# Kernel tuning notes

Hardware: AMD Instinct MI355X
Metric: run time of the kernel (lower is better)

## Reference

```python
import jax, jax.numpy as jnp
import numpy as np

NUM_HEADS = 12
NUM_LANDMARKS = 64
EPS_REG = 1e-4


def setup_inputs() -> dict:
    key = jax.random.key(0)
    k1, k2, k3 = jax.random.split(key, 3)
    B, N, C = 4, 4096, 768
    x = jax.random.normal(k1, (B, N, C), dtype=jnp.float32)
    w_qkv = jax.random.normal(k2, (3 * C, C), dtype=jnp.float32) * (C ** -0.5)
    w_proj = jax.random.normal(k3, (C, C), dtype=jnp.float32) * (C ** -0.5)
    b_proj = jnp.zeros((C,), dtype=jnp.float32)
    return {"x": x, "w_qkv": w_qkv, "w_proj": w_proj, "b_proj": b_proj}


def _landmark_pool(t, m):
    # t: [B, H, N, D]; assumes N % m == 0 (true for chosen shapes)
    B, H, N, D = t.shape
    seg = N // m
    return t.reshape(B, H, m, seg, D).mean(axis=3)


def reference(x, w_qkv, w_proj, b_proj):
    B, N, C = x.shape
    H = NUM_HEADS
    D = C // H
    m = min(NUM_LANDMARKS, N)
    scale = D ** -0.5

    qkv = x @ w_qkv.T                              # [B, N, 3C]
    qkv = qkv.reshape(B, N, 3, H, D).transpose(2, 0, 3, 1, 4)
    q, k, v = qkv[0], qkv[1], qkv[2]               # [B, H, N, D]

    q_lm = _landmark_pool(q, m)                    # [B, H, m, D]
    k_lm = _landmark_pool(k, m)                    # [B, H, m, D]

    attn_q_km = jax.nn.softmax(jnp.einsum('bhnd,bhmd->bhnm', q, k_lm) * scale, axis=-1)
    attn_qm_km = jax.nn.softmax(jnp.einsum('bhld,bhmd->bhlm', q_lm, k_lm) * scale, axis=-1)
    attn_qm_k = jax.nn.softmax(jnp.einsum('bhmd,bhnd->bhmn', q_lm, k) * scale, axis=-1)

    eye = jnp.eye(m, dtype=attn_qm_km.dtype)
    inv_mid = jnp.linalg.inv(attn_qm_km + EPS_REG * eye)   # [B, H, m, m]

    out = attn_q_km @ (inv_mid @ (attn_qm_k @ v))          # [B, H, N, D]
    out = out.transpose(0, 2, 1, 3).reshape(B, N, C)
    out = out @ w_proj.T + b_proj
    return out
```

## Files before the change

### kernel.cpp

```cpp
#include <hip/hip_runtime.h>

typedef unsigned short u16;
typedef __attribute__((ext_vector_type(8))) short bf16x8;
typedef __attribute__((ext_vector_type(8))) unsigned short u16x8;
typedef __attribute__((ext_vector_type(4))) unsigned short u16x4;
typedef __attribute__((ext_vector_type(4))) float f32x4;

#define NB 4
#define NH 12
#define NSEQ 4096
#define NC 768
#define ND 64
#define NM 64
#define NBH 48

__device__ __forceinline__ float b2f(u16 u){ unsigned v = ((unsigned)u)<<16; return __builtin_bit_cast(float, v); }
__device__ __forceinline__ u16 f2b(float f){ unsigned u = __builtin_bit_cast(unsigned, f); u = u + 0x7FFFu + ((u>>16)&1u); return (u16)(u>>16); }
__device__ __forceinline__ void split2(float f, u16& h, u16& l){
  h = f2b(f);
  l = f2b(f - b2f(h));
}

typedef const __attribute__((address_space(1))) unsigned int guint;
typedef __attribute__((address_space(3))) unsigned int luint;
__device__ __forceinline__ void gload16(const void* g, void* l){
  __builtin_amdgcn_global_load_lds((guint*)g, (luint*)l, 16, 0, 0);
}

__device__ __forceinline__ f32x4 mfma16x16(bf16x8 a, bf16x8 b, f32x4 c){
  return __builtin_amdgcn_mfma_f32_16x16x32_bf16(a, b, c, 0, 0, 0);
}

#define NX4 3145728
#define NWQ4 442368
#define NWP4 147456
__global__ __launch_bounds__(256) void k_split3(const float* __restrict__ x, const float* __restrict__ wq,
                                                const float* __restrict__ wp,
                                                u16* __restrict__ xh, u16* __restrict__ xl,
                                                u16* __restrict__ wqh, u16* __restrict__ wql,
                                                u16* __restrict__ wph, u16* __restrict__ wpl){
  int i = blockIdx.x*256 + threadIdx.x;
  const float* src; u16 *dh, *dl; int j;
  if (i < NX4){ src = x; dh = xh; dl = xl; j = i; }
  else if (i < NX4+NWQ4){ src = wq; dh = wqh; dl = wql; j = i - NX4; }
  else if (i < NX4+NWQ4+NWP4){ src = wp; dh = wph; dl = wpl; j = i - NX4 - NWQ4; }
  else return;
  f32x4 v = ((const f32x4*)src)[j];
  u16x4 hh, ll;
  #pragma unroll
  for (int e=0;e<4;++e){ u16 hb, lb; split2(v[e], hb, lb); hh[e]=hb; ll[e]=lb; }
  ((u16x4*)dh)[j] = hh; ((u16x4*)dl)[j] = ll;
}


__global__ __launch_bounds__(256) void k_qkv(const u16* __restrict__ xh, const u16* __restrict__ xl,
                                             const u16* __restrict__ wh, const u16* __restrict__ wl,
                                             u16* __restrict__ qh, u16* __restrict__ ql,
                                             u16* __restrict__ kh, u16* __restrict__ kl,
                                             u16* __restrict__ vTh, u16* __restrict__ vTl,
                                             float* __restrict__ qlmf, float* __restrict__ klmf,
                                             u16* __restrict__ qlmh, u16* __restrict__ qlml,
                                             u16* __restrict__ klmh, u16* __restrict__ klml){
  __shared__ u16 lds[32768];
  const int K = NC;
  int tid = threadIdx.x, wave = tid>>6, lane = tid&63;
  int wm = wave>>1, wn = wave&1;
  int bid = blockIdx.x;
  int swz = (bid&7)*288 + (bid>>3);
  int bx = swz % 18, by = swz / 18;
  int m0 = by*128, n0 = bx*128;
  int srow = lane>>3;
  int scol = ((lane&7) ^ srow)*8;
  const u16* src0; u16* dst0;
  if (wave==0){ src0 = xh + (size_t)m0*K; dst0 = lds; }
  else if (wave==1){ src0 = xl + (size_t)m0*K; dst0 = lds+8192; }
  else if (wave==2){ src0 = wh + (size_t)n0*K; dst0 = lds+16384; }
  else            { src0 = wl + (size_t)n0*K; dst0 = lds+24576; }
  f32x4 acc[4][4] = {};
  for (int k0=0; k0<K; k0+=64){
    #pragma unroll
    for (int it=0; it<16; ++it){
      int r = it*8;
      gload16(&src0[(size_t)(r+srow)*K + k0 + scol], &dst0[r*64]);
    }
    __syncthreads();
    #pragma unroll
    for (int kk=0; kk<2; ++kk){
      int sl = ((kk*4 + (lane>>4)) ^ (lane&7))*8;
      bf16x8 a_h[4], a_l[4], b_h[4], b_l[4];
      #pragma unroll
      for (int i=0;i<4;++i){
        int ro = (wm*64+i*16+(lane&15))*64 + sl;
        a_h[i] = *(const bf16x8*)&lds[ro]; a_l[i] = *(const bf16x8*)&lds[8192+ro];
      }
      #pragma unroll
      for (int j=0;j<4;++j){
        int ro = (wn*64+j*16+(lane&15))*64 + sl;
        b_h[j] = *(const bf16x8*)&lds[16384+ro]; b_l[j] = *(const bf16x8*)&lds[24576+ro];
      }
      #pragma unroll
      for (int i=0;i<4;++i)
        #pragma unroll
        for (int j=0;j<4;++j){
          acc[i][j] = mfma16x16(a_h[i], b_h[j], acc[i][j]);
          acc[i][j] = mfma16x16(a_h[i], b_l[j], acc[i][j]);
          acc[i][j] = mfma16x16(a_l[i], b_h[j], acc[i][j]);
        }
    }
    __syncthreads();
  }
  int rb = (lane>>4)*4, cb = lane&15;
  int b_ = m0>>12, nlo = m0&4095;
  if (n0 < 1536){
    int s = n0/768;
    u16* dh = s ? kh : qh;
    u16* dl = s ? kl : ql;
    float* lmf = s ? klmf : qlmf;
    u16* lmh = s ? klmh : qlmh;
    u16* lml = s ? klml : qlml;
    #pragma unroll
    for (int j=0;j<4;++j){
      int gn = n0 + wn*64 + j*16 + cb;
      int rem = gn - s*768; int hd = rem>>6, d = rem&63;
      #pragma unroll
      for (int i=0;i<4;++i)
        #pragma unroll
        for (int r=0;r<4;++r){
          int n = nlo + wm*64 + i*16 + rb + r;
          size_t idx = (((size_t)(b_*NH + hd))*NSEQ + n)*ND + d;
          u16 hb, lb; split2(acc[i][j][r], hb, lb);
          dh[idx] = hb; dl[idx] = lb;
        }
      float tot = 0.f;
      #pragma unroll
      for (int i=0;i<4;++i)
        #pragma unroll
        for (int r=0;r<4;++r) tot += acc[i][j][r];
      tot += __shfl_xor(tot, 16);
      tot += __shfl_xor(tot, 32);
      if (lane < 16){
        int lseg = (nlo>>6) + wm;
        float mean = tot * (1.f/64.f);
        size_t o = (((size_t)(b_*NH + hd))*NM + lseg)*ND + d;
        lmf[o] = mean;
        u16 hb, lb; split2(mean, hb, lb);
        lmh[o] = hb; lml[o] = lb;
      }
    }
  } else {
    const int TS = 136;
    #pragma unroll
    for (int part=0; part<2; ++part){
      __syncthreads();
      #pragma unroll
      for (int j=0;j<4;++j){
        int dcol = wn*64 + j*16 + cb;
        #pragma unroll
        for (int i=0;i<4;++i)
          #pragma unroll
          for (int r=0;r<4;++r){
            int nrow = wm*64 + i*16 + rb + r;
            u16 hb, lb; split2(acc[i][j][r], hb, lb);
            lds[dcol*TS + nrow] = part ? lb : hb;
          }
      }
      __syncthreads();
      int drow = tid>>1, half = (tid&1)*64;
      int remd = (n0 - 1536) + drow;
      int hd = remd>>6, dd = remd&63;
      u16* dst = (part ? vTl : vTh) + (((size_t)(b_*NH + hd))*ND + dd)*NSEQ + nlo + half;
      const u16* srcl = &lds[drow*TS + half];
      #pragma unroll
      for (int e=0;e<8;++e)
        *(u16x8*)(dst + e*8) = *(const u16x8*)(srcl + e*8);
    }
  }
}

__global__ __launch_bounds__(256) void k_proj(const u16* __restrict__ Hh, const u16* __restrict__ Hl,
                                              const u16* __restrict__ wh, const u16* __restrict__ wl,
                                              const float* __restrict__ bias, float* __restrict__ out){
  __shared__ u16 lds[32768];
  const int K = NC;
  int tid = threadIdx.x, wave = tid>>6, lane = tid&63;
  int wm = wave>>1, wn = wave&1;
  int bid = blockIdx.x;
  int swz = (bid&7)*96 + (bid>>3);
  int bx = swz % 6, by = swz / 6;
  int m0 = by*128, n0 = bx*128;
  int srow = lane>>3;
  int scol = ((lane&7) ^ srow)*8;
  const u16* src0; u16* dst0;
  if (wave==0){ src0 = Hh + (size_t)m0*K; dst0 = lds; }
  else if (wave==1){ src0 = Hl + (size_t)m0*K; dst0 = lds+8192; }
  else if (wave==2){ src0 = wh + (size_t)n0*K; dst0 = lds+16384; }
  else            { src0 = wl + (size_t)n0*K; dst0 = lds+24576; }
  f32x4 acc[4][4] = {};
  for (int k0=0; k0<K; k0+=64){
    #pragma unroll
    for (int it=0; it<16; ++it){
      int r = it*8;
      gload16(&src0[(size_t)(r+srow)*K + k0 + scol], &dst0[r*64]);
    }
    __syncthreads();
    #pragma unroll
    for (int kk=0; kk<2; ++kk){
      int sl = ((kk*4 + (lane>>4)) ^ (lane&7))*8;
      bf16x8 a_h[4], a_l[4], b_h[4], b_l[4];
      #pragma unroll
      for (int i=0;i<4;++i){
        int ro = (wm*64+i*16+(lane&15))*64 + sl;
        a_h[i] = *(const bf16x8*)&lds[ro]; a_l[i] = *(const bf16x8*)&lds[8192+ro];
      }
      #pragma unroll
      for (int j=0;j<4;++j){
        int ro = (wn*64+j*16+(lane&15))*64 + sl;
        b_h[j] = *(const bf16x8*)&lds[16384+ro]; b_l[j] = *(const bf16x8*)&lds[24576+ro];
      }
      #pragma unroll
      for (int i=0;i<4;++i)
        #pragma unroll
        for (int j=0;j<4;++j){
          acc[i][j] = mfma16x16(a_h[i], b_h[j], acc[i][j]);
          acc[i][j] = mfma16x16(a_h[i], b_l[j], acc[i][j]);
          acc[i][j] = mfma16x16(a_l[i], b_h[j], acc[i][j]);
        }
    }
    __syncthreads();
  }
  int rb = (lane>>4)*4, cb = lane&15;
  #pragma unroll
  for (int j=0;j<4;++j){
    int gn = n0 + wn*64 + j*16 + cb;
    float bb = bias[gn];
    #pragma unroll
    for (int i=0;i<4;++i){
      #pragma unroll
      for (int r=0;r<4;++r){
        int gm = m0 + wm*64 + i*16 + rb + r;
        out[(size_t)gm*NC + gn] = acc[i][j][r] + bb;
      }
    }
  }
}

__global__ __launch_bounds__(256) void k_s2(const u16* __restrict__ qlmh, const u16* __restrict__ qlml,
                                            const u16* __restrict__ kh, const u16* __restrict__ kl,
                                            float* __restrict__ s2f, float* __restrict__ stats){
  int chunk = blockIdx.x, bh = blockIdx.y;
  int tid = threadIdx.x, wave = tid>>6, lane = tid&63;
  const u16* Ahp = qlmh + (size_t)bh*NM*ND;
  const u16* Alp = qlml + (size_t)bh*NM*ND;
  const u16* Bhp = kh + (size_t)bh*NSEQ*ND;
  const u16* Blp = kl + (size_t)bh*NSEQ*ND;
  int nbase = chunk*256 + wave*64;
  f32x4 acc[4][4] = {};
  #pragma unroll
  for (int kk=0; kk<2; ++kk){
    int koff = kk*32 + (lane>>4)*8;
    bf16x8 a_h[4], a_l[4], b_h[4], b_l[4];
    #pragma unroll
    for (int i=0;i<4;++i){
      size_t ro = (size_t)(i*16+(lane&15))*ND + koff;
      a_h[i] = *(const bf16x8*)&Ahp[ro]; a_l[i] = *(const bf16x8*)&Alp[ro];
    }
    #pragma unroll
    for (int j=0;j<4;++j){
      size_t ro = (size_t)(nbase + j*16 + (lane&15))*ND + koff;
      b_h[j] = *(const bf16x8*)&Bhp[ro]; b_l[j] = *(const bf16x8*)&Blp[ro];
    }
    #pragma unroll
    for (int i=0;i<4;++i)
      #pragma unroll
      for (int j=0;j<4;++j){
        acc[i][j] = mfma16x16(a_h[i], b_h[j], acc[i][j]);
        acc[i][j] = mfma16x16(a_h[i], b_l[j], acc[i][j]);
        acc[i][j] = mfma16x16(a_l[i], b_h[j], acc[i][j]);
      }
  }
  int rb = (lane>>4)*4, cb = lane&15;
  #pragma unroll
  for (int i=0;i<4;++i)
    #pragma unroll
    for (int j=0;j<4;++j)
      #pragma unroll
      for (int r=0;r<4;++r){
        int l = i*16 + rb + r; int n = nbase + j*16 + cb;
        s2f[((size_t)bh*NM + l)*NSEQ + n] = acc[i][j][r]*0.125f;
      }
  #pragma unroll
  for (int i=0;i<4;++i)
    #pragma unroll
    for (int r=0;r<4;++r){
      float v0 = acc[i][0][r]*0.125f, v1 = acc[i][1][r]*0.125f;
      float v2 = acc[i][2][r]*0.125f, v3 = acc[i][3][r]*0.125f;
      float mx = fmaxf(fmaxf(v0,v1), fmaxf(v2,v3));
      #pragma unroll
      for (int off=1; off<16; off<<=1) mx = fmaxf(mx, __shfl_xor(mx, off));
      float se = __expf(v0-mx)+__expf(v1-mx)+__expf(v2-mx)+__expf(v3-mx);
      #pragma unroll
      for (int off=1; off<16; off<<=1) se += __shfl_xor(se, off);
      if (cb == 0){
        int row = i*16 + rb + r;
        size_t o = ((((size_t)chunk*NBH + bh)*4 + wave)*64 + row)*2;
        stats[o] = mx; stats[o+1] = se;
      }
    }
}

__global__ __launch_bounds__(256) void k_t1(const float* __restrict__ s2f, const float* __restrict__ stats,
                                            const u16* __restrict__ vTh, const u16* __restrict__ vTl,
                                            float* __restrict__ t1p){
  int kb = blockIdx.x, bh = blockIdx.y;
  int tid = threadIdx.x, wave = tid>>6, lane = tid&63;
  int arow = wave*16 + (lane&15);
  float MX = -1e30f;
  for (int c=0;c<16;++c)
    #pragma unroll
    for (int w=0;w<4;++w)
      MX = fmaxf(MX, stats[((((size_t)c*NBH + bh)*4 + w)*64 + arow)*2]);
  float SE = 0.f;
  for (int c=0;c<16;++c)
    #pragma unroll
    for (int w=0;w<4;++w){
      size_t o = ((((size_t)c*NBH + bh)*4 + w)*64 + arow)*2;
      SE += stats[o+1]*__expf(stats[o]-MX);
    }
  float INV = 1.f/SE;
  const float* srow = s2f + ((size_t)bh*NM + arow)*NSEQ;
  const u16* Bh = vTh + (size_t)bh*ND*NSEQ;
  const u16* Bl = vTl + (size_t)bh*ND*NSEQ;
  f32x4 acc[4] = {};
  for (int ks=0; ks<16; ++ks){
    int koff = kb*512 + ks*32 + (lane>>4)*8;
    f32x4 sv0 = *(const f32x4*)&srow[koff];
    f32x4 sv1 = *(const f32x4*)&srow[koff+4];
    bf16x8 a_h, a_l;
    #pragma unroll
    for (int e=0;e<4;++e){
      u16 hb, lb;
      split2(__expf(sv0[e]-MX)*INV, hb, lb); a_h[e]   = (short)hb; a_l[e]   = (short)lb;
      split2(__expf(sv1[e]-MX)*INV, hb, lb); a_h[4+e] = (short)hb; a_l[4+e] = (short)lb;
    }
    #pragma unroll
    for (int j=0;j<4;++j){
      size_t ro = (size_t)(j*16+(lane&15))*NSEQ + koff;
      bf16x8 b_h = *(const bf16x8*)&Bh[ro];
      bf16x8 b_l = *(const bf16x8*)&Bl[ro];
      acc[j] = mfma16x16(a_h, b_h, acc[j]);
      acc[j] = mfma16x16(a_h, b_l, acc[j]);
      acc[j] = mfma16x16(a_l, b_h, acc[j]);
    }
  }
  int rb = (lane>>4)*4, cb = lane&15;
  #pragma unroll
  for (int j=0;j<4;++j)
    #pragma unroll
    for (int r=0;r<4;++r){
      int l = wave*16 + rb + r; int d = j*16 + cb;
      t1p[((size_t)(kb*NBH + bh)*NM + l)*ND + d] = acc[j][r];
    }
}

__global__ __launch_bounds__(256) void k_mid(const float* __restrict__ qlmf, const float* __restrict__ klmf,
                                            const float* __restrict__ t1p,
                                            u16* __restrict__ w2th, u16* __restrict__ w2tl){
  __shared__ float M[64*68];
  __shared__ float T[64*68];
  __shared__ int piv_s;
  int bh = blockIdx.x, tid = threadIdx.x;
  int r = tid>>2, qd = tid&3;
  const float* qrow  = qlmf + (size_t)bh*NM*ND + r*64;
  const float* kbase = klmf + (size_t)bh*NM*ND;
  float qv[64];
  #pragma unroll
  for (int e=0;e<16;++e){
    f32x4 t4 = ((const f32x4*)qrow)[e];
    qv[e*4]=t4[0]; qv[e*4+1]=t4[1]; qv[e*4+2]=t4[2]; qv[e*4+3]=t4[3];
  }
  float sv[16];
  #pragma unroll
  for (int mi=0;mi<16;++mi){
    const float* krow = kbase + (size_t)(qd*16+mi)*64;
    float a = 0.f;
    #pragma unroll
    for (int e=0;e<16;++e){
      f32x4 k4 = ((const f32x4*)krow)[e];
      a += qv[e*4]*k4[0] + qv[e*4+1]*k4[1] + qv[e*4+2]*k4[2] + qv[e*4+3]*k4[3];
    }
    sv[mi] = a*0.125f;
  }
  float mx = sv[0];
  #pragma unroll
  for (int mi=1;mi<16;++mi) mx = fmaxf(mx, sv[mi]);
  mx = fmaxf(mx, __shfl_xor(mx,1)); mx = fmaxf(mx, __shfl_xor(mx,2));
  float sum = 0.f;
  #pragma unroll
  for (int mi=0;mi<16;++mi){ sv[mi] = __expf(sv[mi]-mx); sum += sv[mi]; }
  sum += __shfl_xor(sum,1); sum += __shfl_xor(sum,2);
  float sinv = 1.f/sum;
  #pragma unroll
  for (int mi=0;mi<16;++mi){
    int m = qd*16+mi;
    float p = sv[mi]*sinv;
    if (m == r) p += 1e-4f;
    M[r*68+m] = p;
  }
  #pragma unroll
  for (int q=0;q<4;++q){
    int c = qd*16 + q*4;
    f32x4 a = {};
    #pragma unroll
    for (int kb=0;kb<8;++kb)
      a += *(const f32x4*)&t1p[((size_t)(kb*NBH + bh)*NM + r)*ND + c];
    *(f32x4*)&T[r*68+c] = a;
  }
  __syncthreads();
  for (int kp=0; kp<64; ++kp){
    if (tid < 64){
      float val = (tid >= kp) ? fabsf(M[tid*68+kp]) : -1.f;
      int idx = tid;
      #pragma unroll
      for (int off=32; off; off>>=1){
        float ov = __shfl_xor(val, off); int oi = __shfl_xor(idx, off);
        if (ov > val || (ov == val && oi < idx)){ val = ov; idx = oi; }
      }
      if (tid == 0) piv_s = idx;
    }
    __syncthreads();
    int p = piv_s;
    if (r == kp){
      float pinv = 1.f / M[p*68+kp];
      f32x4 mk[4], mp[4], tk[4], tp_[4];
      #pragma unroll
      for (int q=0;q<4;++q){
        int c = qd*16 + q*4;
        mk[q] = *(const f32x4*)&M[kp*68+c]; mp[q] = *(const f32x4*)&M[p*68+c];
        tk[q] = *(const f32x4*)&T[kp*68+c]; tp_[q] = *(const f32x4*)&T[p*68+c];
      }
      #pragma unroll
      for (int q=0;q<4;++q){
        int c = qd*16 + q*4;
        *(f32x4*)&M[p*68+c] = mk[q];       *(f32x4*)&T[p*68+c] = tk[q];
        *(f32x4*)&M[kp*68+c] = mp[q]*pinv; *(f32x4*)&T[kp*68+c] = tp_[q]*pinv;
      }
    }
    __syncthreads();
    if (r != kp){
      float f = M[r*68+kp];
      #pragma unroll
      for (int q=0;q<4;++q){
        int c = qd*16 + q*4;
        f32x4 pm = *(const f32x4*)&M[kp*68+c];
        f32x4 om = *(const f32x4*)&M[r*68+c];
        *(f32x4*)&M[r*68+c] = om - f*pm;
        f32x4 pt = *(const f32x4*)&T[kp*68+c];
        f32x4 ot = *(const f32x4*)&T[r*68+c];
        *(f32x4*)&T[r*68+c] = ot - f*pt;
      }
    }
    __syncthreads();
  }
  int d = tid>>2, qs = tid&3;
  #pragma unroll
  for (int li=0; li<16; ++li){
    int l = qs*16 + li;
    float xv = T[l*68 + d];
    u16 hb, lb; split2(xv, hb, lb);
    size_t o = ((size_t)bh*ND + d)*NM + l;
    w2th[o] = hb; w2tl[o] = lb;
  }
}

__global__ __launch_bounds__(256) void k_final(const u16* __restrict__ qh, const u16* __restrict__ ql,
                                               const u16* __restrict__ klmh, const u16* __restrict__ klml,
                                               const u16* __restrict__ w2th, const u16* __restrict__ w2tl,
                                               u16* __restrict__ Hh, u16* __restrict__ Hl){
  __shared__ u16 Ph[4*4096], Pl[4*4096];
  int chunk = blockIdx.x, bh = blockIdx.y;
  int b_ = bh/NH, hd = bh - b_*NH;
  int tid = threadIdx.x, wave = tid>>6, lane = tid&63;
  int n0 = chunk*256 + wave*64;
  const u16* qhp = qh + ((size_t)bh*NSEQ + n0)*ND;
  const u16* qlp = ql + ((size_t)bh*NSEQ + n0)*ND;
  const u16* Kh = klmh + (size_t)bh*NM*ND;
  const u16* Kl = klml + (size_t)bh*NM*ND;
  const u16* Wh = w2th + (size_t)bh*ND*NM;
  const u16* Wl = w2tl + (size_t)bh*ND*NM;
  u16* Phw = Ph + wave*4096;
  u16* Plw = Pl + wave*4096;
  f32x4 accs[4][4] = {};
  #pragma unroll
  for (int kk=0; kk<2; ++kk){
    int koff = kk*32 + (lane>>4)*8;
    bf16x8 a_h[4], a_l[4], b_h[4], b_l[4];
    #pragma unroll
    for (int i=0;i<4;++i){
      size_t ro = (size_t)(i*16+(lane&15))*ND + koff;
      a_h[i] = *(const bf16x8*)&qhp[ro]; a_l[i] = *(const bf16x8*)&qlp[ro];
    }
    #pragma unroll
    for (int j=0;j<4;++j){
      size_t ro = (size_t)(j*16+(lane&15))*ND + koff;
      b_h[j] = *(const bf16x8*)&Kh[ro]; b_l[j] = *(const bf16x8*)&Kl[ro];
    }
    #pragma unroll
    for (int i=0;i<4;++i)
      #pragma unroll
      for (int j=0;j<4;++j){
        accs[i][j] = mfma16x16(a_h[i], b_h[j], accs[i][j]);
        accs[i][j] = mfma16x16(a_h[i], b_l[j], accs[i][j]);
        accs[i][j] = mfma16x16(a_l[i], b_h[j], accs[i][j]);
      }
  }
  #pragma unroll
  for (int i=0;i<4;++i)
    #pragma unroll
    for (int j=0;j<4;++j) accs[i][j] *= 0.125f;
  int rb = (lane>>4)*4, cb = lane&15;
  #pragma unroll
  for (int i=0;i<4;++i){
    #pragma unroll
    for (int r=0;r<4;++r){
      float mx = -1e30f;
      #pragma unroll
      for (int j=0;j<4;++j) mx = fmaxf(mx, accs[i][j][r]);
      #pragma unroll
      for (int off=1; off<16; off<<=1) mx = fmaxf(mx, __shfl_xor(mx, off));
      float e[4]; float sum = 0.f;
      #pragma unroll
      for (int j=0;j<4;++j){ e[j] = __expf(accs[i][j][r]-mx); sum += e[j]; }
      #pragma unroll
      for (int off=1; off<16; off<<=1) sum += __shfl_xor(sum, off);
      float inv = 1.f/sum;
      int row = i*16 + rb + r;
      #pragma unroll
      for (int j=0;j<4;++j){
        u16 hb, lb; split2(e[j]*inv, hb, lb);
        int col = j*16 + cb;
        int scol = (((col>>3) ^ (row&7))<<3) | (col&7);
        Phw[row*64 + scol] = hb;
        Plw[row*64 + scol] = lb;
      }
    }
  }
  __syncthreads();
  f32x4 acco[4][4] = {};
  #pragma unroll
  for (int kk=0; kk<2; ++kk){
    int koff = kk*32 + (lane>>4)*8;
    int sl = ((kk*4 + (lane>>4)) ^ (lane&7))*8;
    bf16x8 a_h[4], a_l[4], b_h[4], b_l[4];
    #pragma unroll
    for (int i=0;i<4;++i){
      int ro = (i*16+(lane&15))*64 + sl;
      a_h[i] = *(const bf16x8*)&Phw[ro]; a_l[i] = *(const bf16x8*)&Plw[ro];
    }
    #pragma unroll
    for (int j=0;j<4;++j){
      size_t ro = (size_t)(j*16+(lane&15))*64 + koff;
      b_h[j] = *(const bf16x8*)&Wh[ro]; b_l[j] = *(const bf16x8*)&Wl[ro];
    }
    #pragma unroll
    for (int i=0;i<4;++i)
      #pragma unroll
      for (int j=0;j<4;++j){
        acco[i][j] = mfma16x16(a_h[i], b_h[j], acco[i][j]);
        acco[i][j] = mfma16x16(a_h[i], b_l[j], acco[i][j]);
        acco[i][j] = mfma16x16(a_l[i], b_h[j], acco[i][j]);
      }
  }
  #pragma unroll
  for (int i=0;i<4;++i)
    #pragma unroll
    for (int j=0;j<4;++j)
      #pragma unroll
      for (int r=0;r<4;++r){
        int n = n0 + i*16 + rb + r;
        int d = j*16 + cb;
        size_t o = ((size_t)(b_*NSEQ + n))*NC + hd*64 + d;
        u16 hb, lb; split2(acco[i][j][r], hb, lb);
        Hh[o] = hb; Hl[o] = lb;
      }
}

__global__ void k_sent(float* out){ out[0] = 1.0e9f; }

#define OFF_QH     0ull
#define OFF_QL     25165824ull
#define OFF_KH     50331648ull
#define OFF_KL     75497472ull
#define OFF_VTH    100663296ull
#define OFF_VTL    125829120ull
#define OFF_S2     150994944ull
#define OFF_QLMF   201326592ull
#define OFF_KLMF   202113024ull
#define OFF_QLMH   202899456ull
#define OFF_QLML   203292672ull
#define OFF_KLMH   203685888ull
#define OFF_KLML   204079104ull
#define OFF_W2TH   204472320ull
#define OFF_W2TL   204865536ull
#define OFF_T1P    205258752ull
#define OFF_WQH    211550208ull
#define OFF_WQL    215089152ull
#define OFF_WPH    218628096ull
#define OFF_WPL    219807744ull
#define WS_NEEDED  220987392ull

extern "C" void kernel_launch(void* const* d_in, const int* in_sizes, int n_in,
                              void* d_out, int out_size, void* d_ws, size_t ws_size,
                              hipStream_t stream){
  const float* x     = (const float*)d_in[0];
  const float* wqkv  = (const float*)d_in[1];
  const float* wproj = (const float*)d_in[2];
  const float* bproj = (const float*)d_in[3];
  float* out = (float*)d_out;
  char* ws = (char*)d_ws;
  if (ws_size < WS_NEEDED){ k_sent<<<1,1,0,stream>>>(out); return; }
  u16* qh = (u16*)(ws + OFF_QH);  u16* ql = (u16*)(ws + OFF_QL);
  u16* kh = (u16*)(ws + OFF_KH);  u16* kl = (u16*)(ws + OFF_KL);
  u16* vTh = (u16*)(ws + OFF_VTH); u16* vTl = (u16*)(ws + OFF_VTL);
  u16* xh = (u16*)(ws + OFF_S2);
  u16* xl = (u16*)(ws + OFF_S2 + 25165824ull);
  float* s2f = (float*)(ws + OFF_S2);
  u16* Hh = (u16*)(ws + OFF_S2);
  u16* Hl = (u16*)(ws + OFF_S2 + 25165824ull);
  float* qlmf = (float*)(ws + OFF_QLMF);
  float* klmf = (float*)(ws + OFF_KLMF);
  u16* qlmh = (u16*)(ws + OFF_QLMH); u16* qlml = (u16*)(ws + OFF_QLML);
  u16* klmh = (u16*)(ws + OFF_KLMH); u16* klml = (u16*)(ws + OFF_KLML);
  u16* w2th = (u16*)(ws + OFF_W2TH); u16* w2tl = (u16*)(ws + OFF_W2TL);
  float* t1p = (float*)(ws + OFF_T1P);
  u16* wqh = (u16*)(ws + OFF_WQH); u16* wql = (u16*)(ws + OFF_WQL);
  u16* wph = (u16*)(ws + OFF_WPH); u16* wpl = (u16*)(ws + OFF_WPL);
  float* stats = (float*)(ws + OFF_WQH);

  k_split3   <<<14592, 256, 0, stream>>>(x, wqkv, wproj, xh, xl, wqh, wql, wph, wpl);
  k_qkv      <<<2304, 256, 0, stream>>>(xh, xl, wqh, wql, qh, ql, kh, kl, vTh, vTl,
                                        qlmf, klmf, qlmh, qlml, klmh, klml);
  k_s2       <<<dim3(16,48),  256, 0, stream>>>(qlmh, qlml, kh, kl, s2f, stats);
  k_t1       <<<dim3(8,48),   256, 0, stream>>>(s2f, stats, vTh, vTl, t1p);
  k_mid      <<<48,           256, 0, stream>>>(qlmf, klmf, t1p, w2th, w2tl);
  k_final    <<<dim3(16,48),  256, 0, stream>>>(qh, ql, klmh, klml, w2th, w2tl, Hh, Hl);
  k_proj     <<<768,          256, 0, stream>>>(Hh, Hl, wph, wpl, bproj, out);
}
```

Baseline: 495.3 us.

## Rewrite QKV GEMM as 256x256 tile with 4-stage async LDS pipeline

Replaces the 128x128, 4-wave QKV GEMM with a 256x256-tile, 8-wave kernel. The three split-bf16 products become 72 k-steps (three segments of 24) that stream through a 4-buffer LDS ring with explicit vmcnt waits, barriers and setprio around the MFMAs. The goal is to overlap global loads with MFMA work and raise data reuse per loaded tile, cutting memory stalls and sync overhead. The epilogue is reworked for the larger tile: landmark means are computed per 64-row half, and the V transpose goes through LDS in two passes. The cost is more LDS, more registers and fewer blocks (576), which may hurt occupancy and tail balance.

```diff
diff --git a/kernel.cpp b/kernel.cpp
--- a/kernel.cpp
+++ b/kernel.cpp
@@ -52,62 +52,79 @@
   ((u16x4*)dh)[j] = hh; ((u16x4*)dl)[j] = ll;
 }
 
-
-__global__ __launch_bounds__(256) void k_qkv(const u16* __restrict__ xh, const u16* __restrict__ xl,
-                                             const u16* __restrict__ wh, const u16* __restrict__ wl,
-                                             u16* __restrict__ qh, u16* __restrict__ ql,
-                                             u16* __restrict__ kh, u16* __restrict__ kl,
-                                             u16* __restrict__ vTh, u16* __restrict__ vTl,
-                                             float* __restrict__ qlmf, float* __restrict__ klmf,
-                                             u16* __restrict__ qlmh, u16* __restrict__ qlml,
-                                             u16* __restrict__ klmh, u16* __restrict__ klml){
-  __shared__ u16 lds[32768];
-  const int K = NC;
+__global__ __launch_bounds__(512,2) void k_qkv8(const u16* __restrict__ xh, const u16* __restrict__ xl,
+                                                const u16* __restrict__ wh, const u16* __restrict__ wl,
+                                                u16* __restrict__ qh, u16* __restrict__ ql,
+                                                u16* __restrict__ kh, u16* __restrict__ kl,
+                                                u16* __restrict__ vTh, u16* __restrict__ vTl,
+                                                float* __restrict__ qlmf, float* __restrict__ klmf,
+                                                u16* __restrict__ qlmh, u16* __restrict__ qlml,
+                                                u16* __restrict__ klmh, u16* __restrict__ klml){
+  __shared__ u16 lds[65536];
   int tid = threadIdx.x, wave = tid>>6, lane = tid&63;
-  int wm = wave>>1, wn = wave&1;
+  int wm = wave>>2, wn = wave&3;
   int bid = blockIdx.x;
-  int swz = (bid&7)*288 + (bid>>3);
-  int bx = swz % 18, by = swz / 18;
-  int m0 = by*128, n0 = bx*128;
-  int srow = lane>>3;
-  int scol = ((lane&7) ^ srow)*8;
-  const u16* src0; u16* dst0;
-  if (wave==0){ src0 = xh + (size_t)m0*K; dst0 = lds; }
-  else if (wave==1){ src0 = xl + (size_t)m0*K; dst0 = lds+8192; }
-  else if (wave==2){ src0 = wh + (size_t)n0*K; dst0 = lds+16384; }
-  else            { src0 = wl + (size_t)n0*K; dst0 = lds+24576; }
-  f32x4 acc[4][4] = {};
-  for (int k0=0; k0<K; k0+=64){
-    #pragma unroll
-    for (int it=0; it<16; ++it){
-      int r = it*8;
-      gload16(&src0[(size_t)(r+srow)*K + k0 + scol], &dst0[r*64]);
-    }
-    __syncthreads();
-    #pragma unroll
-    for (int kk=0; kk<2; ++kk){
-      int sl = ((kk*4 + (lane>>4)) ^ (lane&7))*8;
-      bf16x8 a_h[4], a_l[4], b_h[4], b_l[4];
-      #pragma unroll
-      for (int i=0;i<4;++i){
-        int ro = (wm*64+i*16+(lane&15))*64 + sl;
-        a_h[i] = *(const bf16x8*)&lds[ro]; a_l[i] = *(const bf16x8*)&lds[8192+ro];
-      }
-      #pragma unroll
-      for (int j=0;j<4;++j){
-        int ro = (wn*64+j*16+(lane&15))*64 + sl;
-        b_h[j] = *(const bf16x8*)&lds[16384+ro]; b_l[j] = *(const bf16x8*)&lds[24576+ro];
-      }
-      #pragma unroll
-      for (int i=0;i<4;++i)
-        #pragma unroll
-        for (int j=0;j<4;++j){
-          acc[i][j] = mfma16x16(a_h[i], b_h[j], acc[i][j]);
-          acc[i][j] = mfma16x16(a_h[i], b_l[j], acc[i][j]);
-          acc[i][j] = mfma16x16(a_l[i], b_h[j], acc[i][j]);
-        }
-    }
-    __syncthreads();
+  int swz = (bid&7)*72 + (bid>>3);
+  int bx = swz % 9, by = swz / 9;
+  int m0 = by*256, n0 = bx*256;
+  int trow = tid>>2, tslot = tid&3;
+  int gs = (tslot ^ ((trow>>1)&3))*8;
+  const u16* aXh0 = xh + (size_t)(m0+trow)*NC + gs;
+  const u16* aXh1 = xh + (size_t)(m0+128+trow)*NC + gs;
+  const u16* aXl0 = xl + (size_t)(m0+trow)*NC + gs;
+  const u16* aXl1 = xl + (size_t)(m0+128+trow)*NC + gs;
+  const u16* bWh0 = wh + (size_t)(n0+trow)*NC + gs;
+  const u16* bWh1 = wh + (size_t)(n0+128+trow)*NC + gs;
+  const u16* bWl0 = wl + (size_t)(n0+trow)*NC + gs;
+  const u16* bWl1 = wl + (size_t)(n0+128+trow)*NC + gs;
+  auto stageA = [&](int tt){
+    int seg = tt/24, kc = (tt%24)*32, bo = (tt&3)*16384;
+    const u16* p0 = (seg==2)? aXl0 : aXh0;
+    const u16* p1 = (seg==2)? aXl1 : aXh1;
+    gload16(p0+kc, &lds[bo + wave*512]);
+    gload16(p1+kc, &lds[bo + 4096 + wave*512]);
+  };
+  auto stageB = [&](int tt){
+    int seg = tt/24, kc = (tt%24)*32, bo = (tt&3)*16384;
+    const u16* p0 = (seg==1)? bWl0 : bWh0;
+    const u16* p1 = (seg==1)? bWl1 : bWh1;
+    gload16(p0+kc, &lds[bo + 8192 + wave*512]);
+    gload16(p1+kc, &lds[bo + 8192 + 4096 + wave*512]);
+  };
+  int la = lane&15;
+  int sl = ((lane>>4) ^ ((la>>1)&3))*8;
+  f32x4 acc[8][4] = {};
+  stageA(0); stageB(0); stageA(1); stageB(1); stageA(2); stageB(2);
+  for (int t=0; t<72; ++t){
+    if (t < 70)      asm volatile("s_waitcnt vmcnt(8)" ::: "memory");
+    else if (t==70)  asm volatile("s_waitcnt vmcnt(4)" ::: "memory");
+    else             asm volatile("s_waitcnt vmcnt(0)" ::: "memory");
+    __builtin_amdgcn_s_barrier();
+    __builtin_amdgcn_sched_barrier(0);
+    int bo = (t&3)*16384;
+    bool st = (t <= 68);
+    bf16x8 av[4], bv[4];
+    #pragma unroll
+    for (int j=0;j<4;++j) bv[j] = *(const bf16x8*)&lds[bo + 8192 + (wn*64 + j*16 + la)*32 + sl];
+    #pragma unroll
+    for (int i=0;i<4;++i) av[i] = *(const bf16x8*)&lds[bo + (wm*128 + i*16 + la)*32 + sl];
+    if (st) stageA(t+3);
+    __builtin_amdgcn_s_setprio(1);
+    #pragma unroll
+    for (int i=0;i<4;++i)
+      #pragma unroll
+      for (int j=0;j<4;++j) acc[i][j] = mfma16x16(av[i], bv[j], acc[i][j]);
+    __builtin_amdgcn_s_setprio(0);
+    __builtin_amdgcn_s_barrier();
+    #pragma unroll
+    for (int i=0;i<4;++i) av[i] = *(const bf16x8*)&lds[bo + (wm*128 + 64 + i*16 + la)*32 + sl];
+    if (st) stageB(t+3);
+    __builtin_amdgcn_s_setprio(1);
+    #pragma unroll
+    for (int i=0;i<4;++i)
+      #pragma unroll
+      for (int j=0;j<4;++j) acc[4+i][j] = mfma16x16(av[i], bv[j], acc[4+i][j]);
+    __builtin_amdgcn_s_setprio(0);
   }
   int rb = (lane>>4)*4, cb = lane&15;
   int b_ = m0>>12, nlo = m0&4095;
@@ -123,56 +140,64 @@
       int gn = n0 + wn*64 + j*16 + cb;
       int rem = gn - s*768; int hd = rem>>6, d = rem&63;
       #pragma unroll
-      for (int i=0;i<4;++i)
-        #pragma unroll
-        for (int r=0;r<4;++r){
-          int n = nlo + wm*64 + i*16 + rb + r;
-          size_t idx = (((size_t)(b_*NH + hd))*NSEQ + n)*ND + d;
-          u16 hb, lb; split2(acc[i][j][r], hb, lb);
-          dh[idx] = hb; dl[idx] = lb;
-        }
-      float tot = 0.f;
-      #pragma unroll
-      for (int i=0;i<4;++i)
-        #pragma unroll
-        for (int r=0;r<4;++r) tot += acc[i][j][r];
-      tot += __shfl_xor(tot, 16);
-      tot += __shfl_xor(tot, 32);
-      if (lane < 16){
-        int lseg = (nlo>>6) + wm;
-        float mean = tot * (1.f/64.f);
-        size_t o = (((size_t)(b_*NH + hd))*NM + lseg)*ND + d;
-        lmf[o] = mean;
-        u16 hb, lb; split2(mean, hb, lb);
-        lmh[o] = hb; lml[o] = lb;
-      }
-    }
-  } else {
-    const int TS = 136;
-    #pragma unroll
-    for (int part=0; part<2; ++part){
-      __syncthreads();
-      #pragma unroll
-      for (int j=0;j<4;++j){
-        int dcol = wn*64 + j*16 + cb;
+      for (int qi=0; qi<2; ++qi){
+        float tot = 0.f;
         #pragma unroll
         for (int i=0;i<4;++i)
           #pragma unroll
           for (int r=0;r<4;++r){
-            int nrow = wm*64 + i*16 + rb + r;
-            u16 hb, lb; split2(acc[i][j][r], hb, lb);
-            lds[dcol*TS + nrow] = part ? lb : hb;
+            float v = acc[qi*4+i][j][r];
+            int n = nlo + wm*128 + qi*64 + i*16 + rb + r;
+            size_t idx = (((size_t)(b_*NH + hd))*NSEQ + n)*ND + d;
+            u16 hb, lb; split2(v, hb, lb);
+            dh[idx] = hb; dl[idx] = lb;
+            tot += v;
           }
-      }
-      __syncthreads();
-      int drow = tid>>1, half = (tid&1)*64;
-      int remd = (n0 - 1536) + drow;
-      int hd = remd>>6, dd = remd&63;
-      u16* dst = (part ? vTl : vTh) + (((size_t)(b_*NH + hd))*ND + dd)*NSEQ + nlo + half;
-      const u16* srcl = &lds[drow*TS + half];
-      #pragma unroll
-      for (int e=0;e<8;++e)
-        *(u16x8*)(dst + e*8) = *(const u16x8*)(srcl + e*8);
+        tot += __shfl_xor(tot, 16);
+        tot += __shfl_xor(tot, 32);
+        if (lane < 16){
+          int lseg = (nlo>>6) + wm*2 + qi;
+          float mean = tot * (1.f/64.f);
+          size_t o = (((size_t)(b_*NH + hd))*NM + lseg)*ND + d;
+          lmf[o] = mean;
+          u16 hb, lb; split2(mean, hb, lb);
+          lmh[o] = hb; lml[o] = lb;
+        }
+      }
+    }
+  } else {
+    #pragma unroll
+    for (int part=0; part<2; ++part){
+      #pragma unroll
+      for (int p=0; p<2; ++p){
+        __syncthreads();
+        if ((wn>>1) == p){
+          int dbase = (wn&1)*64;
+          #pragma unroll
+          for (int j=0;j<4;++j){
+            int dcol = dbase + j*16 + cb;
+            #pragma unroll
+            for (int qi=0;qi<2;++qi)
+              #pragma unroll
+              for (int i=0;i<4;++i)
+                #pragma unroll
+                for (int r=0;r<4;++r){
+                  int row = wm*128 + qi*64 + i*16 + rb + r;
+                  u16 hb, lb; split2(acc[qi*4+i][j][r], hb, lb);
+                  lds[dcol*264 + row] = part ? lb : hb;
+                }
+          }
+        }
+        __syncthreads();
+        int dloc = tid>>2, seg = tid&3;
+        int vcol = (n0 - 1536) + p*128 + dloc;
+        int hd = vcol>>6, dd = vcol&63;
+        u16* dst = (part ? vTl : vTh) + (((size_t)(b_*NH + hd))*ND + dd)*NSEQ + nlo + seg*64;
+        const u16* srcl = &lds[dloc*264 + seg*64];
+        #pragma unroll
+        for (int e=0;e<8;++e)
+          *(u16x8*)(dst + e*8) = *(const u16x8*)(srcl + e*8);
+      }
     }
   }
 }
@@ -637,8 +662,8 @@
   float* stats = (float*)(ws + OFF_WQH);
 
   k_split3   <<<14592, 256, 0, stream>>>(x, wqkv, wproj, xh, xl, wqh, wql, wph, wpl);
-  k_qkv      <<<2304, 256, 0, stream>>>(xh, xl, wqh, wql, qh, ql, kh, kl, vTh, vTl,
-                                        qlmf, klmf, qlmh, qlml, klmh, klml);
+  k_qkv8     <<<576, 512, 0, stream>>>(xh, xl, wqh, wql, qh, ql, kh, kl, vTh, vTl,
+                                       qlmf, klmf, qlmh, qlml, klmh, klml);
   k_s2       <<<dim3(16,48),  256, 0, stream>>>(qlmh, qlml, kh, kl, s2f, stats);
   k_t1       <<<dim3(8,48),   256, 0, stream>>>(s2f, stats, vTh, vTl, t1p);
   k_mid      <<<48,           256, 0, stream>>>(qlmf, klmf, t1p, w2th, w2tl);
```

Result: slower. 586.0 us (+18.3%).

## Fuse landmark-query scores, softmax and PV into one online-softmax kernel

Applied to the files above, without the earlier changes.

Replaces the two-pass k_s2/k_t1 pipeline with a flash-attention style kernel that computes q_lm·k scores, applies an online softmax and accumulates P·V per 512-column chunk. Probabilities are staged in swizzled shared memory instead of writing a full fp32 score matrix to global memory. Per-chunk max/sum statistics go to a small buffer, and k_mid merges the partial outputs with rescaling. This removes one launch and the large score write and re-read, at the cost of fewer blocks (384) doing serial chunk work.

```diff
diff --git a/kernel.cpp b/kernel.cpp
--- a/kernel.cpp
+++ b/kernel.cpp
@@ -244,126 +244,106 @@
   }
 }
 
-__global__ __launch_bounds__(256) void k_s2(const u16* __restrict__ qlmh, const u16* __restrict__ qlml,
-                                            const u16* __restrict__ kh, const u16* __restrict__ kl,
-                                            float* __restrict__ s2f, float* __restrict__ stats){
-  int chunk = blockIdx.x, bh = blockIdx.y;
-  int tid = threadIdx.x, wave = tid>>6, lane = tid&63;
-  const u16* Ahp = qlmh + (size_t)bh*NM*ND;
-  const u16* Alp = qlml + (size_t)bh*NM*ND;
-  const u16* Bhp = kh + (size_t)bh*NSEQ*ND;
-  const u16* Blp = kl + (size_t)bh*NSEQ*ND;
-  int nbase = chunk*256 + wave*64;
-  f32x4 acc[4][4] = {};
-  #pragma unroll
-  for (int kk=0; kk<2; ++kk){
-    int koff = kk*32 + (lane>>4)*8;
-    bf16x8 a_h[4], a_l[4], b_h[4], b_l[4];
-    #pragma unroll
-    for (int i=0;i<4;++i){
-      size_t ro = (size_t)(i*16+(lane&15))*ND + koff;
-      a_h[i] = *(const bf16x8*)&Ahp[ro]; a_l[i] = *(const bf16x8*)&Alp[ro];
-    }
-    #pragma unroll
-    for (int j=0;j<4;++j){
-      size_t ro = (size_t)(nbase + j*16 + (lane&15))*ND + koff;
-      b_h[j] = *(const bf16x8*)&Bhp[ro]; b_l[j] = *(const bf16x8*)&Blp[ro];
-    }
-    #pragma unroll
-    for (int i=0;i<4;++i)
-      #pragma unroll
-      for (int j=0;j<4;++j){
-        acc[i][j] = mfma16x16(a_h[i], b_h[j], acc[i][j]);
-        acc[i][j] = mfma16x16(a_h[i], b_l[j], acc[i][j]);
-        acc[i][j] = mfma16x16(a_l[i], b_h[j], acc[i][j]);
-      }
-  }
-  int rb = (lane>>4)*4, cb = lane&15;
-  #pragma unroll
-  for (int i=0;i<4;++i)
-    #pragma unroll
-    for (int j=0;j<4;++j)
-      #pragma unroll
-      for (int r=0;r<4;++r){
-        int l = i*16 + rb + r; int n = nbase + j*16 + cb;
-        s2f[((size_t)bh*NM + l)*NSEQ + n] = acc[i][j][r]*0.125f;
-      }
-  #pragma unroll
-  for (int i=0;i<4;++i)
-    #pragma unroll
-    for (int r=0;r<4;++r){
-      float v0 = acc[i][0][r]*0.125f, v1 = acc[i][1][r]*0.125f;
-      float v2 = acc[i][2][r]*0.125f, v3 = acc[i][3][r]*0.125f;
-      float mx = fmaxf(fmaxf(v0,v1), fmaxf(v2,v3));
-      #pragma unroll
-      for (int off=1; off<16; off<<=1) mx = fmaxf(mx, __shfl_xor(mx, off));
-      float se = __expf(v0-mx)+__expf(v1-mx)+__expf(v2-mx)+__expf(v3-mx);
-      #pragma unroll
-      for (int off=1; off<16; off<<=1) se += __shfl_xor(se, off);
-      if (cb == 0){
-        int row = i*16 + rb + r;
-        size_t o = ((((size_t)chunk*NBH + bh)*4 + wave)*64 + row)*2;
-        stats[o] = mx; stats[o+1] = se;
-      }
-    }
-}
-
-__global__ __launch_bounds__(256) void k_t1(const float* __restrict__ s2f, const float* __restrict__ stats,
-                                            const u16* __restrict__ vTh, const u16* __restrict__ vTl,
-                                            float* __restrict__ t1p){
+__global__ __launch_bounds__(256) void k_fat1(const u16* __restrict__ qlmh, const u16* __restrict__ qlml,
+                                              const u16* __restrict__ kh, const u16* __restrict__ kl,
+                                              const u16* __restrict__ vTh, const u16* __restrict__ vTl,
+                                              float* __restrict__ t1p, float* __restrict__ st2){
+  __shared__ u16 Ph[4096], Pl[4096];
   int kb = blockIdx.x, bh = blockIdx.y;
   int tid = threadIdx.x, wave = tid>>6, lane = tid&63;
-  int arow = wave*16 + (lane&15);
-  float MX = -1e30f;
-  for (int c=0;c<16;++c)
-    #pragma unroll
-    for (int w=0;w<4;++w)
-      MX = fmaxf(MX, stats[((((size_t)c*NBH + bh)*4 + w)*64 + arow)*2]);
-  float SE = 0.f;
-  for (int c=0;c<16;++c)
-    #pragma unroll
-    for (int w=0;w<4;++w){
-      size_t o = ((((size_t)c*NBH + bh)*4 + w)*64 + arow)*2;
-      SE += stats[o+1]*__expf(stats[o]-MX);
-    }
-  float INV = 1.f/SE;
-  const float* srow = s2f + ((size_t)bh*NM + arow)*NSEQ;
-  const u16* Bh = vTh + (size_t)bh*ND*NSEQ;
-  const u16* Bl = vTl + (size_t)bh*ND*NSEQ;
-  f32x4 acc[4] = {};
-  for (int ks=0; ks<16; ++ks){
-    int koff = kb*512 + ks*32 + (lane>>4)*8;
-    f32x4 sv0 = *(const f32x4*)&srow[koff];
-    f32x4 sv1 = *(const f32x4*)&srow[koff+4];
-    bf16x8 a_h, a_l;
-    #pragma unroll
-    for (int e=0;e<4;++e){
-      u16 hb, lb;
-      split2(__expf(sv0[e]-MX)*INV, hb, lb); a_h[e]   = (short)hb; a_l[e]   = (short)lb;
-      split2(__expf(sv1[e]-MX)*INV, hb, lb); a_h[4+e] = (short)hb; a_l[4+e] = (short)lb;
-    }
-    #pragma unroll
-    for (int j=0;j<4;++j){
-      size_t ro = (size_t)(j*16+(lane&15))*NSEQ + koff;
-      bf16x8 b_h = *(const bf16x8*)&Bh[ro];
-      bf16x8 b_l = *(const bf16x8*)&Bl[ro];
-      acc[j] = mfma16x16(a_h, b_h, acc[j]);
-      acc[j] = mfma16x16(a_h, b_l, acc[j]);
-      acc[j] = mfma16x16(a_l, b_h, acc[j]);
-    }
-  }
-  int rb = (lane>>4)*4, cb = lane&15;
+  int la = lane&15, hi = lane>>4;
+  u16* Pwh = Ph + wave*1024;
+  u16* Pwl = Pl + wave*1024;
+  bf16x8 qa_h[2], qa_l[2];
+  #pragma unroll
+  for (int kk=0;kk<2;++kk){
+    size_t ro = ((size_t)bh*NM + wave*16 + la)*ND + kk*32 + hi*8;
+    qa_h[kk] = *(const bf16x8*)&qlmh[ro];
+    qa_l[kk] = *(const bf16x8*)&qlml[ro];
+  }
+  float m_[4] = {-1e30f,-1e30f,-1e30f,-1e30f};
+  float l_[4] = {0.f,0.f,0.f,0.f};
+  f32x4 pv[4] = {};
+  for (int ch=0; ch<8; ++ch){
+    int nbase = kb*512 + ch*64;
+    f32x4 s_[4] = {};
+    #pragma unroll
+    for (int kk=0;kk<2;++kk){
+      int koff = kk*32 + hi*8;
+      #pragma unroll
+      for (int j=0;j<4;++j){
+        size_t ro = ((size_t)bh*NSEQ + nbase + j*16 + la)*ND + koff;
+        bf16x8 b_h = *(const bf16x8*)&kh[ro];
+        bf16x8 b_l = *(const bf16x8*)&kl[ro];
+        s_[j] = mfma16x16(qa_h[kk], b_h, s_[j]);
+        s_[j] = mfma16x16(qa_h[kk], b_l, s_[j]);
+        s_[j] = mfma16x16(qa_l[kk], b_h, s_[j]);
+      }
+    }
+    #pragma unroll
+    for (int r=0;r<4;++r){
+      float v0=s_[0][r]*0.125f, v1=s_[1][r]*0.125f, v2=s_[2][r]*0.125f, v3=s_[3][r]*0.125f;
+      float mx = fmaxf(fmaxf(v0,v1), fmaxf(v2,v3));
+      #pragma unroll
+      for (int off=1; off<16; off<<=1) mx = fmaxf(mx, __shfl_xor(mx, off));
+      float mn = fmaxf(m_[r], mx);
+      float fr = __expf(m_[r] - mn);
+      float p0=__expf(v0-mn), p1=__expf(v1-mn), p2=__expf(v2-mn), p3=__expf(v3-mn);
+      float se = p0+p1+p2+p3;
+      #pragma unroll
+      for (int off=1; off<16; off<<=1) se += __shfl_xor(se, off);
+      l_[r] = l_[r]*fr + se;
+      m_[r] = mn;
+      pv[0][r]*=fr; pv[1][r]*=fr; pv[2][r]*=fr; pv[3][r]*=fr;
+      int row = hi*4 + r;
+      float pj0=p0, pj1=p1, pj2=p2, pj3=p3;
+      #pragma unroll
+      for (int j=0;j<4;++j){
+        float pval = (j==0)?pj0:(j==1)?pj1:(j==2)?pj2:pj3;
+        u16 hb, lb; split2(pval, hb, lb);
+        int col = j*16 + la;
+        int scol = (((col>>3) ^ (row&7))<<3) | (col&7);
+        Pwh[row*64 + scol] = hb;
+        Pwl[row*64 + scol] = lb;
+      }
+    }
+    #pragma unroll
+    for (int kk=0;kk<2;++kk){
+      int sl2 = ((kk*4 + hi) ^ (la&7))*8;
+      bf16x8 pa_h = *(const bf16x8*)&Pwh[la*64 + sl2];
+      bf16x8 pa_l = *(const bf16x8*)&Pwl[la*64 + sl2];
+      int koff = nbase + kk*32 + hi*8;
+      #pragma unroll
+      for (int j=0;j<4;++j){
+        size_t ro = ((size_t)bh*ND + j*16 + la)*NSEQ + koff;
+        bf16x8 b_h = *(const bf16x8*)&vTh[ro];
+        bf16x8 b_l = *(const bf16x8*)&vTl[ro];
+        pv[j] = mfma16x16(pa_h, b_h, pv[j]);
+        pv[j] = mfma16x16(pa_h, b_l, pv[j]);
+        pv[j] = mfma16x16(pa_l, b_h, pv[j]);
+      }
+    }
+  }
   #pragma unroll
   for (int j=0;j<4;++j)
     #pragma unroll
     for (int r=0;r<4;++r){
-      int l = wave*16 + rb + r; int d = j*16 + cb;
-      t1p[((size_t)(kb*NBH + bh)*NM + l)*ND + d] = acc[j][r];
-    }
+      int row = wave*16 + hi*4 + r;
+      int d = j*16 + la;
+      t1p[(((size_t)(kb*NBH + bh))*NM + row)*ND + d] = pv[j][r];
+    }
+  if (la == 0){
+    #pragma unroll
+    for (int r=0;r<4;++r){
+      int row = wave*16 + hi*4 + r;
+      size_t o = (((size_t)(kb*NBH + bh))*NM + row)*2;
+      st2[o] = m_[r]; st2[o+1] = l_[r];
+    }
+  }
 }
 
 __global__ __launch_bounds__(256) void k_mid(const float* __restrict__ qlmf, const float* __restrict__ klmf,
-                                            const float* __restrict__ t1p,
+                                            const float* __restrict__ t1p, const float* __restrict__ st2,
                                             u16* __restrict__ w2th, u16* __restrict__ w2tl){
   __shared__ float M[64*68];
   __shared__ float T[64*68];
@@ -406,14 +386,27 @@
     if (m == r) p += 1e-4f;
     M[r*68+m] = p;
   }
+  float Mx = -1e30f;
+  #pragma unroll
+  for (int kb2=0;kb2<8;++kb2)
+    Mx = fmaxf(Mx, st2[(((size_t)(kb2*NBH + bh))*NM + r)*2]);
+  float L = 0.f; float wsc[8];
+  #pragma unroll
+  for (int kb2=0;kb2<8;++kb2){
+    size_t o = (((size_t)(kb2*NBH + bh))*NM + r)*2;
+    float w = __expf(st2[o] - Mx);
+    wsc[kb2] = w;
+    L += w * st2[o+1];
+  }
+  float Linv = 1.f / L;
   #pragma unroll
   for (int q=0;q<4;++q){
     int c = qd*16 + q*4;
     f32x4 a = {};
     #pragma unroll
-    for (int kb=0;kb<8;++kb)
-      a += *(const f32x4*)&t1p[((size_t)(kb*NBH + bh)*NM + r)*ND + c];
-    *(f32x4*)&T[r*68+c] = a;
+    for (int kb2=0;kb2<8;++kb2)
+      a += wsc[kb2] * *(const f32x4*)&t1p[((size_t)(kb2*NBH + bh)*NM + r)*ND + c];
+    *(f32x4*)&T[r*68+c] = a * Linv;
   }
   __syncthreads();
   for (int kp=0; kp<64; ++kp){
@@ -623,7 +616,6 @@
   u16* vTh = (u16*)(ws + OFF_VTH); u16* vTl = (u16*)(ws + OFF_VTL);
   u16* xh = (u16*)(ws + OFF_S2);
   u16* xl = (u16*)(ws + OFF_S2 + 25165824ull);
-  float* s2f = (float*)(ws + OFF_S2);
   u16* Hh = (u16*)(ws + OFF_S2);
   u16* Hl = (u16*)(ws + OFF_S2 + 25165824ull);
   float* qlmf = (float*)(ws + OFF_QLMF);
@@ -634,14 +626,13 @@
   float* t1p = (float*)(ws + OFF_T1P);
   u16* wqh = (u16*)(ws + OFF_WQH); u16* wql = (u16*)(ws + OFF_WQL);
   u16* wph = (u16*)(ws + OFF_WPH); u16* wpl = (u16*)(ws + OFF_WPL);
-  float* stats = (float*)(ws + OFF_WQH);
+  float* st2 = (float*)(ws + OFF_WQH);
 
   k_split3   <<<14592, 256, 0, stream>>>(x, wqkv, wproj, xh, xl, wqh, wql, wph, wpl);
   k_qkv      <<<2304, 256, 0, stream>>>(xh, xl, wqh, wql, qh, ql, kh, kl, vTh, vTl,
                                         qlmf, klmf, qlmh, qlml, klmh, klml);
-  k_s2       <<<dim3(16,48),  256, 0, stream>>>(qlmh, qlml, kh, kl, s2f, stats);
-  k_t1       <<<dim3(8,48),   256, 0, stream>>>(s2f, stats, vTh, vTl, t1p);
-  k_mid      <<<48,           256, 0, stream>>>(qlmf, klmf, t1p, w2th, w2tl);
+  k_fat1     <<<dim3(8,48),   256, 0, stream>>>(qlmh, qlml, kh, kl, vTh, vTl, t1p, st2);
+  k_mid      <<<48,           256, 0, stream>>>(qlmf, klmf, t1p, st2, w2th, w2tl);
   k_final    <<<dim3(16,48),  256, 0, stream>>>(qh, ql, klmh, klml, w2th, w2tl, Hh, Hl);
   k_proj     <<<768,          256, 0, stream>>>(Hh, Hl, wph, wpl, bproj, out);
 }
```

New measurement: 486.7 us. Within noise of the previous version (-1.7%).
